# Optimization experiments

Measured on AMD Instinct MI355X. Metric: run time of the kernel, lower is better.

The kernel has to match this reference:

```python
import jax, jax.numpy as jnp
import numpy as np
import jax.lax as lax

H, D, C, CS, NS, OW, PD = 8, 64, 512, 64, 5, 8, 1
MAX_LR = 0.1
KCONV = 4


def short_conv(x, w, b):
    # x: (B,T,Din) -> causal depthwise conv over time
    B, T, Din = x.shape
    xc = jnp.transpose(x, (0, 2, 1))
    xc = jnp.pad(xc, ((0, 0), (0, 0), (KCONV - 1, 0)))
    xc = lax.conv_general_dilated(xc, w, window_strides=(1,), padding='VALID',
                                  dimension_numbers=('NCW', 'OIW', 'NCW'),
                                  feature_group_count=Din)
    xc = xc + b[:, jnp.newaxis]
    return jnp.transpose(xc, (0, 2, 1))


def linear_scan(h_init, gates, inputs):
    # h_t = gate_t * h_{t-1} + input_t ; gates: (B,cs,H), inputs: (B,cs,H,...)
    extra = inputs.ndim - gates.ndim
    g = gates.reshape(gates.shape + (1,) * extra)
    first = g[:, 0:1] * h_init[:, jnp.newaxis] + inputs[:, 0:1]
    mod_in = jnp.concatenate([first, inputs[:, 1:]], axis=1)
    mod_g = jnp.concatenate([jnp.zeros_like(g[:, 0:1]), g[:, 1:]], axis=1)

    def assoc(a, bb):
        ga, xa = a
        gb, xb = bb
        return (ga * gb, gb * xa + xb)

    _, h_all = lax.associative_scan(assoc, (mod_g, mod_in), axis=1)
    return h_all, h_all[:, -1]


def omega_aggregate(u, gamma, w):
    cs = u.shape[1]
    cum = jnp.cumsum(gamma * u, axis=1)
    if w >= cs:
        return cum
    shifted = jnp.concatenate([jnp.zeros_like(cum[:, :w]), cum[:, :-w]], axis=1)
    return cum - shifted


def polar_express(S, steps):
    # Newton-Schulz quintic orthogonalization (Muon/Polar-Express coefficients)
    a, b, c = 3.4445, -4.7750, 2.0315
    n = jnp.sqrt(jnp.sum(S * S, axis=(-2, -1), keepdims=True))
    X = S / (n * 1.01 + 1e-7)
    for _ in range(steps):
        A = X @ jnp.swapaxes(X, -2, -1)
        X = a * X + (b * A + c * (A @ A)) @ X
    return X


def rms_norm(x):
    ms = jnp.mean(x * x, axis=-1, keepdims=True)
    return x * lax.rsqrt(ms + 1e-6)


def atlas_forward(x, Wq, Wk, Wv, Wproj, conv_q_w, conv_q_b, conv_k_w, conv_k_b,
                  conv_v_w, conv_v_b, ga_w, ga_b, ge_w, ge_b, gt_w, gt_b,
                  gg_w, gg_b, poly_coeffs, ln_gamma, W1_init, rg_w):
    B, T, _ = x.shape
    q = short_conv(x @ Wq.T, conv_q_w, conv_q_b).reshape(B, T, H, D)
    k = short_conv(x @ Wk.T, conv_k_w, conv_k_b).reshape(B, T, H, D)
    v = short_conv(x @ Wv.T, conv_v_w, conv_v_b).reshape(B, T, H, D)

    def phi(z):
        r = poly_coeffs[0] * z
        zp = z
        for i in range(1, PD):
            zp = zp * z
            r = r + poly_coeffs[i] * zp
        return r

    q, k = phi(q), phi(k)

    alpha = jax.nn.sigmoid(x @ ga_w.T + ga_b)          # (B,T,H) memory retention
    eta = MAX_LR * jax.nn.sigmoid(x @ ge_w.T + ge_b)   # learning rate
    theta = jax.nn.sigmoid(x @ gt_w.T + gt_b)          # momentum decay
    gamma = jax.nn.sigmoid(x @ gg_w.T + gg_b)          # omega context gate

    nC = T // CS

    def chunk(z):
        return jnp.moveaxis(z.reshape(B, nC, CS, *z.shape[2:]), 1, 0)

    q_ch, k_ch, v_ch = chunk(q), chunk(k), chunk(v)
    a_ch = chunk(alpha)[..., None]
    e_ch = chunk(eta)[..., None]
    t_ch = chunk(theta)[..., None]
    g_ch = chunk(gamma)[..., None]

    M0 = jnp.broadcast_to(W1_init, (B, H, D, D))
    S0 = jnp.zeros((B, H, D, D), x.dtype)

    def step(carry, inp):
        M, S = carry
        q_c, k_c, v_c, a_c, e_c, t_c, g_c = inp
        pred = jnp.einsum('bhvk,bchk->bchv', M, k_c)
        err = pred - v_c
        u = (2.0 / D) * jnp.einsum('bchv,bchk->bchvk', err, k_c)
        u = omega_aggregate(u, g_c[..., None], OW)
        mom_in = -(e_c[..., None] * u)
        chunk_S, S = linear_scan(S, jnp.squeeze(t_c, -1), mom_in)
        chunk_S_orth = polar_express(chunk_S, NS)
        M_all, M = linear_scan(M, jnp.squeeze(a_c, -1), chunk_S_orth)
        y_c = jnp.einsum('bchvk,bchk->bchv', M_all, q_c)
        return (M, S), y_c

    (_, _), y = lax.scan(step, (M0, S0), (q_ch, k_ch, v_ch, a_ch, e_ch, t_ch, g_ch))
    y = jnp.moveaxis(y, 0, 1).reshape(B, T, H, D)
    y = rms_norm(y) * (1.0 + ln_gamma)
    rg = jax.nn.sigmoid(x @ rg_w.T)          # (B,T,H) retrieve gate
    y = y * rg[..., None]
    return y.reshape(B, T, H * D) @ Wproj.T


def setup_inputs() -> dict:
    key = jax.random.key(0)
    ks = jax.random.split(key, 24)
    B, T = 2, 1024
    Din = H * D

    def lin(k, o, i):
        return jax.random.normal(k, (o, i), jnp.float32) * (1.0 / np.sqrt(i))

    bound = float(np.sqrt(6.0 / (D + D)))
    return dict(
        x=jax.random.normal(ks[0], (B, T, C), jnp.float32),
        Wq=lin(ks[1], Din, C), Wk=lin(ks[2], Din, C), Wv=lin(ks[3], Din, C),
        Wproj=lin(ks[4], C, Din),
        conv_q_w=jax.random.normal(ks[5], (Din, 1, KCONV), jnp.float32) * 0.02,
        conv_q_b=jnp.zeros(Din, jnp.float32),
        conv_k_w=jax.random.normal(ks[6], (Din, 1, KCONV), jnp.float32) * 0.02,
        conv_k_b=jnp.zeros(Din, jnp.float32),
        conv_v_w=jax.random.normal(ks[7], (Din, 1, KCONV), jnp.float32) * 0.02,
        conv_v_b=jnp.zeros(Din, jnp.float32),
        ga_w=lin(ks[8], H, C), ga_b=jnp.zeros(H, jnp.float32),
        ge_w=lin(ks[9], H, C), ge_b=jnp.zeros(H, jnp.float32),
        gt_w=lin(ks[10], H, C), gt_b=jnp.zeros(H, jnp.float32),
        gg_w=lin(ks[11], H, C), gg_b=jnp.zeros(H, jnp.float32),
        poly_coeffs=jnp.ones(PD, jnp.float32),
        ln_gamma=jnp.zeros((H, D), jnp.float32),
        W1_init=jax.random.uniform(ks[12], (H, D, D), jnp.float32, -bound, bound),
        rg_w=lin(ks[13], H, C),
    )


def reference(x, Wq, Wk, Wv, Wproj, conv_q_w, conv_q_b, conv_k_w, conv_k_b,
              conv_v_w, conv_v_b, ga_w, ga_b, ge_w, ge_b, gt_w, gt_b,
              gg_w, gg_b, poly_coeffs, ln_gamma, W1_init, rg_w):
    return atlas_forward(x, Wq, Wk, Wv, Wproj, conv_q_w, conv_q_b, conv_k_w,
                         conv_k_b, conv_v_w, conv_v_b, ga_w, ga_b, ge_w, ge_b,
                         gt_w, gt_b, gg_w, gg_b, poly_coeffs, ln_gamma,
                         W1_init, rg_w)
```

## Files before the change

kernel.cpp:

```cpp
#include <hip/hip_runtime.h>

#define B_ 2
#define T_ 1024
#define H_ 8
#define D_ 64
#define PPAD 68

typedef __attribute__((ext_vector_type(8))) short s8v;
typedef __attribute__((ext_vector_type(4))) short s4v;
typedef __attribute__((ext_vector_type(4))) float f4v;

__device__ __forceinline__ short f2bf(float f) {
  unsigned u = __float_as_uint(f);
  u += 0x7fffu + ((u >> 16) & 1u);
  return (short)(u >> 16);
}
__device__ __forceinline__ float bf2f(short s) {
  return __uint_as_float(((unsigned)(unsigned short)s) << 16);
}
__device__ __forceinline__ float sigm(float v) { return 1.0f / (1.0f + __expf(-v)); }

#define MFMA(a, b, c) __builtin_amdgcn_mfma_f32_16x16x32_bf16((a), (b), (c), 0, 0, 0)

__global__ __launch_bounds__(256) void gemm_bt(const float* __restrict__ A,
    const float* __restrict__ Bw, float* __restrict__ Co,
    int M, int N, int K) {
  __shared__ short Ash[64][40], Asl[64][40];
  __shared__ short Bsh[64][40], Bsl[64][40];
  const int tid = threadIdx.x;
  const int lane = tid & 63;
  const int wv = tid >> 6;
  const int wr = (wv >> 1) * 32;
  const int wc = (wv & 1) * 32;
  const int m0 = blockIdx.x * 64;
  const int n0 = blockIdx.y * 64;
  const int ldr = tid >> 2;
  const int ldc = (tid & 3) * 8;
  const int l15 = lane & 15;
  const int kq = (lane >> 4) * 8;
  f4v acc[2][2];
#pragma unroll
  for (int i = 0; i < 2; ++i)
#pragma unroll
    for (int j = 0; j < 2; ++j)
#pragma unroll
      for (int r = 0; r < 4; ++r) acc[i][j][r] = 0.0f;
  const float* ap = A + (size_t)(m0 + ldr) * K + ldc;
  const float* bp = Bw + (size_t)(n0 + ldr) * K + ldc;
  for (int kt = 0; kt < K; kt += 32) {
    float4 av0 = *(const float4*)(ap + kt);
    float4 av1 = *(const float4*)(ap + kt + 4);
    float4 bv0 = *(const float4*)(bp + kt);
    float4 bv1 = *(const float4*)(bp + kt + 4);
    float af[8] = {av0.x, av0.y, av0.z, av0.w, av1.x, av1.y, av1.z, av1.w};
    float bf[8] = {bv0.x, bv0.y, bv0.z, bv0.w, bv1.x, bv1.y, bv1.z, bv1.w};
    s8v ah, al, bh, bl;
#pragma unroll
    for (int i = 0; i < 8; ++i) {
      short h = f2bf(af[i]); ah[i] = h; al[i] = f2bf(af[i] - bf2f(h));
      h = f2bf(bf[i]); bh[i] = h; bl[i] = f2bf(bf[i] - bf2f(h));
    }
    __syncthreads();
    *(s8v*)&Ash[ldr][ldc] = ah; *(s8v*)&Asl[ldr][ldc] = al;
    *(s8v*)&Bsh[ldr][ldc] = bh; *(s8v*)&Bsl[ldr][ldc] = bl;
    __syncthreads();
    s8v a0h = *(const s8v*)&Ash[wr + l15][kq];
    s8v a1h = *(const s8v*)&Ash[wr + 16 + l15][kq];
    s8v b0h = *(const s8v*)&Bsh[wc + l15][kq];
    s8v b1h = *(const s8v*)&Bsh[wc + 16 + l15][kq];
    s8v a0l = *(const s8v*)&Asl[wr + l15][kq];
    s8v a1l = *(const s8v*)&Asl[wr + 16 + l15][kq];
    s8v b0l = *(const s8v*)&Bsl[wc + l15][kq];
    s8v b1l = *(const s8v*)&Bsl[wc + 16 + l15][kq];
    acc[0][0] = MFMA(a0h, b0h, acc[0][0]);
    acc[0][1] = MFMA(a0h, b1h, acc[0][1]);
    acc[1][0] = MFMA(a1h, b0h, acc[1][0]);
    acc[1][1] = MFMA(a1h, b1h, acc[1][1]);
    acc[0][0] = MFMA(a0h, b0l, acc[0][0]);
    acc[0][1] = MFMA(a0h, b1l, acc[0][1]);
    acc[1][0] = MFMA(a1h, b0l, acc[1][0]);
    acc[1][1] = MFMA(a1h, b1l, acc[1][1]);
    acc[0][0] = MFMA(a0l, b0h, acc[0][0]);
    acc[0][1] = MFMA(a0l, b1h, acc[0][1]);
    acc[1][0] = MFMA(a1l, b0h, acc[1][0]);
    acc[1][1] = MFMA(a1l, b1h, acc[1][1]);
  }
#pragma unroll
  for (int m2 = 0; m2 < 2; ++m2)
#pragma unroll
    for (int n2 = 0; n2 < 2; ++n2)
#pragma unroll
      for (int r = 0; r < 4; ++r) {
        int row = m0 + wr + m2 * 16 + (lane >> 4) * 4 + r;
        int col = n0 + wc + n2 * 16 + l15;
        Co[(size_t)row * N + col] = acc[m2][n2][r];
      }
}

__global__ __launch_bounds__(256) void gemm_qkv(const float* __restrict__ A,
    const float* __restrict__ Wq, const float* __restrict__ Wk,
    const float* __restrict__ Wv,
    float* __restrict__ xq, float* __restrict__ xk, float* __restrict__ xv) {
  __shared__ short Ash[64][40], Asl[64][40];
  __shared__ short Bsh[64][40], Bsl[64][40];
  const int sel = blockIdx.y >> 3;
  const float* Bw = sel == 0 ? Wq : (sel == 1 ? Wk : Wv);
  float* Co = sel == 0 ? xq : (sel == 1 ? xk : xv);
  const int tid = threadIdx.x;
  const int lane = tid & 63;
  const int wv = tid >> 6;
  const int wr = (wv >> 1) * 32;
  const int wc = (wv & 1) * 32;
  const int m0 = blockIdx.x * 64;
  const int n0 = (blockIdx.y & 7) * 64;
  const int ldr = tid >> 2;
  const int ldc = (tid & 3) * 8;
  const int l15 = lane & 15;
  const int kq = (lane >> 4) * 8;
  f4v acc[2][2];
#pragma unroll
  for (int i = 0; i < 2; ++i)
#pragma unroll
    for (int j = 0; j < 2; ++j)
#pragma unroll
      for (int r = 0; r < 4; ++r) acc[i][j][r] = 0.0f;
  const float* ap = A + (size_t)(m0 + ldr) * 512 + ldc;
  const float* bp = Bw + (size_t)(n0 + ldr) * 512 + ldc;
  for (int kt = 0; kt < 512; kt += 32) {
    float4 av0 = *(const float4*)(ap + kt);
    float4 av1 = *(const float4*)(ap + kt + 4);
    float4 bv0 = *(const float4*)(bp + kt);
    float4 bv1 = *(const float4*)(bp + kt + 4);
    float af[8] = {av0.x, av0.y, av0.z, av0.w, av1.x, av1.y, av1.z, av1.w};
    float bf[8] = {bv0.x, bv0.y, bv0.z, bv0.w, bv1.x, bv1.y, bv1.z, bv1.w};
    s8v ah, al, bh, bl;
#pragma unroll
    for (int i = 0; i < 8; ++i) {
      short h = f2bf(af[i]); ah[i] = h; al[i] = f2bf(af[i] - bf2f(h));
      h = f2bf(bf[i]); bh[i] = h; bl[i] = f2bf(bf[i] - bf2f(h));
    }
    __syncthreads();
    *(s8v*)&Ash[ldr][ldc] = ah; *(s8v*)&Asl[ldr][ldc] = al;
    *(s8v*)&Bsh[ldr][ldc] = bh; *(s8v*)&Bsl[ldr][ldc] = bl;
    __syncthreads();
    s8v a0h = *(const s8v*)&Ash[wr + l15][kq];
    s8v a1h = *(const s8v*)&Ash[wr + 16 + l15][kq];
    s8v b0h = *(const s8v*)&Bsh[wc + l15][kq];
    s8v b1h = *(const s8v*)&Bsh[wc + 16 + l15][kq];
    s8v a0l = *(const s8v*)&Asl[wr + l15][kq];
    s8v a1l = *(const s8v*)&Asl[wr + 16 + l15][kq];
    s8v b0l = *(const s8v*)&Bsl[wc + l15][kq];
    s8v b1l = *(const s8v*)&Bsl[wc + 16 + l15][kq];
    acc[0][0] = MFMA(a0h, b0h, acc[0][0]);
    acc[0][1] = MFMA(a0h, b1h, acc[0][1]);
    acc[1][0] = MFMA(a1h, b0h, acc[1][0]);
    acc[1][1] = MFMA(a1h, b1h, acc[1][1]);
    acc[0][0] = MFMA(a0h, b0l, acc[0][0]);
    acc[0][1] = MFMA(a0h, b1l, acc[0][1]);
    acc[1][0] = MFMA(a1h, b0l, acc[1][0]);
    acc[1][1] = MFMA(a1h, b1l, acc[1][1]);
    acc[0][0] = MFMA(a0l, b0h, acc[0][0]);
    acc[0][1] = MFMA(a0l, b1h, acc[0][1]);
    acc[1][0] = MFMA(a1l, b0h, acc[1][0]);
    acc[1][1] = MFMA(a1l, b1h, acc[1][1]);
  }
#pragma unroll
  for (int m2 = 0; m2 < 2; ++m2)
#pragma unroll
    for (int n2 = 0; n2 < 2; ++n2)
#pragma unroll
      for (int r = 0; r < 4; ++r) {
        int row = m0 + wr + m2 * 16 + (lane >> 4) * 4 + r;
        int col = n0 + wc + n2 * 16 + l15;
        Co[(size_t)row * 512 + col] = acc[m2][n2][r];
      }
}

__global__ __launch_bounds__(256) void conv3_k(
    const float* __restrict__ xq, const float* __restrict__ xk,
    const float* __restrict__ xv,
    const float* __restrict__ cqw, const float* __restrict__ cqb,
    const float* __restrict__ ckw, const float* __restrict__ ckb,
    const float* __restrict__ cvw, const float* __restrict__ cvb,
    const float* __restrict__ pc,
    float* __restrict__ qb, float* __restrict__ kb, float* __restrict__ vb) {
  const int s = blockIdx.x >> 12;
  const int idx = ((blockIdx.x & 4095) << 8) + threadIdx.x;
  const float* in = s == 0 ? xq : (s == 1 ? xk : xv);
  const float* w  = s == 0 ? cqw : (s == 1 ? ckw : cvw);
  const float* bs = s == 0 ? cqb : (s == 1 ? ckb : cvb);
  float* o        = s == 0 ? qb : (s == 1 ? kb : vb);
  const int d = idx & 511;
  const int bt = idx >> 9;
  const int t = bt & (T_ - 1);
  float acc = bs[d];
#pragma unroll
  for (int j = 0; j < 4; ++j) {
    int tt = t - 3 + j;
    if (tt >= 0) acc += w[d * 4 + j] * in[(size_t)(bt - 3 + j) * 512 + d];
  }
  float sc = (s < 2) ? pc[0] : 1.0f;
  o[idx] = sc * acc;
}

__global__ __launch_bounds__(256) void gates_k(const float* __restrict__ x,
    const float* __restrict__ gaw, const float* __restrict__ gab,
    const float* __restrict__ gew, const float* __restrict__ geb,
    const float* __restrict__ gtw, const float* __restrict__ gtb,
    const float* __restrict__ ggw, const float* __restrict__ ggb,
    const float* __restrict__ rgw,
    float* __restrict__ alpha, float* __restrict__ eta,
    float* __restrict__ theta, float* __restrict__ gam, float* __restrict__ rg) {
  int wv = threadIdx.x >> 6, lane = threadIdx.x & 63;
  int bt = blockIdx.x * 4 + wv;
  float xr[8];
#pragma unroll
  for (int i = 0; i < 8; ++i) xr[i] = x[(size_t)bt * 512 + i * 64 + lane];
  for (int h = 0; h < 8; ++h) {
    float s0 = 0, s1 = 0, s2 = 0, s3 = 0, s4 = 0;
#pragma unroll
    for (int i = 0; i < 8; ++i) {
      float xv = xr[i];
      int o = h * 512 + i * 64 + lane;
      s0 += xv * gaw[o];
      s1 += xv * gew[o];
      s2 += xv * gtw[o];
      s3 += xv * ggw[o];
      s4 += xv * rgw[o];
    }
#pragma unroll
    for (int off = 32; off >= 1; off >>= 1) {
      s0 += __shfl_xor(s0, off);
      s1 += __shfl_xor(s1, off);
      s2 += __shfl_xor(s2, off);
      s3 += __shfl_xor(s3, off);
      s4 += __shfl_xor(s4, off);
    }
    if (lane == 0) {
      size_t o = (size_t)bt * 8 + h;
      alpha[o] = sigm(s0 + gab[h]);
      eta[o]   = 0.1f * sigm(s1 + geb[h]);
      theta[o] = sigm(s2 + gtb[h]);
      gam[o]   = sigm(s3 + ggb[h]);
      rg[o]    = sigm(s4);
    }
  }
}

__global__ __launch_bounds__(256) void init_carry(const float* __restrict__ w1,
    float* __restrict__ Mc, float* __restrict__ Sc) {
  int idx = blockIdx.x * 256 + threadIdx.x;
  Mc[idx] = w1[idx & 32767];
  Sc[idx] = 0.0f;
}

__global__ __launch_bounds__(256) void chunk_a(
    const float* __restrict__ kb, const float* __restrict__ vb,
    const float* __restrict__ eta, const float* __restrict__ theta,
    const float* __restrict__ gam,
    const float* __restrict__ Mc, float* __restrict__ Sc,
    float* __restrict__ chS, int ci) {
  __shared__ float KT[64][65];
  __shared__ float errl[4][68];
  __shared__ float Ml[4][64];
  __shared__ float ge_[64], gt_[64], gg_[64];
  const int tid = threadIdx.x;
  const int bh = blockIdx.x >> 4;
  const int vs = blockIdx.x & 15;
  const int b = bh >> 3, h = bh & 7;
  const int v0 = vs * 4;
  const int t0 = ci * 64;
  const int lane = tid & 63, q4 = tid >> 6;
  for (int it = 0; it < 16; ++it) {
    int c = it * 4 + q4;
    KT[lane][c] = kb[((size_t)(b * T_ + t0 + c) * H_ + h) * 64 + lane];
  }
  if (tid < 64) {
    size_t gi = (size_t)(b * T_ + t0 + tid) * H_ + h;
    ge_[tid] = eta[gi]; gt_[tid] = theta[gi]; gg_[tid] = gam[gi];
  }
  Ml[q4][lane] = Mc[((size_t)bh * 64 + v0 + q4) * 64 + lane];
  __syncthreads();
  {
    int c = lane, vr = q4;
    float p = 0.0f;
#pragma unroll
    for (int k2 = 0; k2 < 64; ++k2) p += KT[k2][c] * Ml[vr][k2];
    float vv = vb[((size_t)(b * T_ + t0 + c) * H_ + h) * 64 + v0 + vr];
    errl[vr][c] = p - vv;
  }
  __syncthreads();
  {
    const int kk = lane, vr = q4, v = v0 + vr;
    float S = Sc[((size_t)bh * 64 + v) * 64 + kk];
    float ring[8];
    float cum = 0.0f;
    float* out = chS + ((size_t)(b << 6) * 8 + h) * 4096 + (size_t)v * 64 + kk;
    for (int c8 = 0; c8 < 8; ++c8) {
#pragma unroll
      for (int j = 0; j < 8; ++j) {
        int c = c8 * 8 + j;
        float u = 0.03125f * errl[vr][c] * KT[kk][c];
        float gu = gg_[c] * u;
        cum += gu;
        if (c8 > 0) cum -= ring[j];
        ring[j] = gu;
        float mom = -ge_[c] * cum;
        S = gt_[c] * S + mom;
        out[(size_t)c * 32768] = S;
      }
    }
    Sc[((size_t)bh * 64 + v) * 64 + kk] = S;
  }
}

__device__ __forceinline__ s8v ld8(const short* p) {
  s4v lo = *(const s4v*)p;
  s4v hi = *(const s4v*)(p + 4);
  s8v r;
  r[0] = lo[0]; r[1] = lo[1]; r[2] = lo[2]; r[3] = lo[3];
  r[4] = hi[0]; r[5] = hi[1]; r[6] = hi[2]; r[7] = hi[3];
  return r;
}

__device__ __forceinline__ void mm8(const short (*Ah)[PPAD], const short (*Al)[PPAD],
    const short (*Bh)[PPAD], const short (*Bl)[PPAD],
    int wr, int wc, int l15, int kq, int sp, f4v acc[2]) {
#pragma unroll
  for (int kt = 0; kt < 64; kt += 32) {
    s8v ah = ld8(&Ah[wr + l15][kt + kq]);
    s8v b0h = ld8(&Bh[wc + l15][kt + kq]);
    s8v b1h = ld8(&Bh[wc + 16 + l15][kt + kq]);
    acc[0] = MFMA(ah, b0h, acc[0]);
    acc[1] = MFMA(ah, b1h, acc[1]);
    if (sp) {
      s8v al_ = ld8(&Al[wr + l15][kt + kq]);
      s8v b0l = ld8(&Bl[wc + l15][kt + kq]);
      s8v b1l = ld8(&Bl[wc + 16 + l15][kt + kq]);
      acc[0] = MFMA(ah, b0l, acc[0]);
      acc[1] = MFMA(ah, b1l, acc[1]);
      acc[0] = MFMA(al_, b0h, acc[0]);
      acc[1] = MFMA(al_, b1h, acc[1]);
    }
  }
}

__global__ __launch_bounds__(512, 6) void polar_k(float* __restrict__ cs) {
  __shared__ short Xh[64][PPAD], Xl[64][PPAD];
  __shared__ short XTh[64][PPAD], XTl[64][PPAD];
  __shared__ short Zh[64][PPAD], Zl[64][PPAD];
  __shared__ float red[8];
  const int tid = threadIdx.x;
  const int lane = tid & 63;
  const int wv = tid >> 6;
  const int wr = (wv >> 1) * 16;
  const int wc = (wv & 1) * 32;
  const int l15 = lane & 15;
  const int q4 = lane >> 4;
  const int kq = q4 * 8;
  const int rr0 = wr + q4 * 4;
  float* base = cs + (size_t)blockIdx.x * 4096;
  float xr[2][4];
  float ss = 0.0f;
#pragma unroll
  for (int n2 = 0; n2 < 2; ++n2)
#pragma unroll
    for (int r = 0; r < 4; ++r) {
      float v = base[(rr0 + r) * 64 + wc + n2 * 16 + l15];
      xr[n2][r] = v;
      ss += v * v;
    }
#pragma unroll
  for (int off = 32; off >= 1; off >>= 1) ss += __shfl_xor(ss, off);
  if (lane == 0) red[wv] = ss;
  __syncthreads();
  float tot = red[0] + red[1] + red[2] + red[3] + red[4] + red[5] + red[6] + red[7];
  float scale = 1.0f / (sqrtf(tot) * 1.01f + 1e-7f);
#pragma unroll
  for (int n2 = 0; n2 < 2; ++n2) {
    const int cc = wc + n2 * 16 + l15;
    s4v hv, lv;
#pragma unroll
    for (int r = 0; r < 4; ++r) {
      float xv = xr[n2][r] * scale;
      xr[n2][r] = xv;
      short hh = f2bf(xv);
      short ll = f2bf(xv - bf2f(hh));
      hv[r] = hh; lv[r] = ll;
      Xh[rr0 + r][cc] = hh;
      Xl[rr0 + r][cc] = ll;
    }
    *(s4v*)&XTh[cc][rr0] = hv;
    *(s4v*)&XTl[cc][rr0] = lv;
  }
  __syncthreads();

  for (int it = 0; it < 5; ++it) {
    const int sp = (it < 4);
    f4v at[2];
#pragma unroll
    for (int n2 = 0; n2 < 2; ++n2)
#pragma unroll
      for (int r = 0; r < 4; ++r) at[n2][r] = 0.0f;
    mm8(XTh, XTl, XTh, XTl, wr, wc, l15, kq, sp, at);
#pragma unroll
    for (int n2 = 0; n2 < 2; ++n2) {
      const int cc = wc + n2 * 16 + l15;
      s4v hv, lv;
#pragma unroll
      for (int r = 0; r < 4; ++r) {
        float a = at[n2][r];
        short hh = f2bf(a);
        hv[r] = hh; lv[r] = f2bf(a - bf2f(hh));
      }
      *(s4v*)&Zh[cc][rr0] = hv;
      if (sp) *(s4v*)&Zl[cc][rr0] = lv;
    }
    __syncthreads();
    f4v a2[2];
#pragma unroll
    for (int n2 = 0; n2 < 2; ++n2)
#pragma unroll
      for (int r = 0; r < 4; ++r) a2[n2][r] = 0.0f;
    mm8(Zh, Zl, Zh, Zl, wr, wc, l15, kq, sp, a2);
    float zt[2][4];
#pragma unroll
    for (int n2 = 0; n2 < 2; ++n2)
#pragma unroll
      for (int r = 0; r < 4; ++r)
        zt[n2][r] = -4.7750f * at[n2][r] + 2.0315f * a2[n2][r];
    __syncthreads();
#pragma unroll
    for (int n2 = 0; n2 < 2; ++n2) {
      const int cc = wc + n2 * 16 + l15;
      s4v hv, lv;
#pragma unroll
      for (int r = 0; r < 4; ++r) {
        float zv = zt[n2][r];
        short hh = f2bf(zv);
        hv[r] = hh; lv[r] = f2bf(zv - bf2f(hh));
      }
      *(s4v*)&Zh[cc][rr0] = hv;
      if (sp) *(s4v*)&Zl[cc][rr0] = lv;
    }
    __syncthreads();
    f4v q3[2];
#pragma unroll
    for (int n2 = 0; n2 < 2; ++n2)
#pragma unroll
      for (int r = 0; r < 4; ++r) q3[n2][r] = 0.0f;
    mm8(Xh, Xl, Zh, Zl, wr, wc, l15, kq, sp, q3);
#pragma unroll
    for (int n2 = 0; n2 < 2; ++n2)
#pragma unroll
      for (int r = 0; r < 4; ++r)
        xr[n2][r] = 3.4445f * xr[n2][r] + q3[n2][r];
    if (it < 4) {
      __syncthreads();
      const int slo = (it < 3);
#pragma unroll
      for (int n2 = 0; n2 < 2; ++n2) {
        const int cc = wc + n2 * 16 + l15;
        s4v hv, lv;
#pragma unroll
        for (int r = 0; r < 4; ++r) {
          float xv = xr[n2][r];
          short hh = f2bf(xv);
          short ll = f2bf(xv - bf2f(hh));
          hv[r] = hh; lv[r] = ll;
          Xh[rr0 + r][cc] = hh;
          if (slo) Xl[rr0 + r][cc] = ll;
        }
        *(s4v*)&XTh[cc][rr0] = hv;
        if (slo) *(s4v*)&XTl[cc][rr0] = lv;
      }
      __syncthreads();
    }
  }
#pragma unroll
  for (int n2 = 0; n2 < 2; ++n2)
#pragma unroll
    for (int r = 0; r < 4; ++r)
      base[(rr0 + r) * 64 + wc + n2 * 16 + l15] = xr[n2][r];
}

__global__ __launch_bounds__(256) void chunk_ca(
    const float* __restrict__ qb, const float* __restrict__ kb,
    const float* __restrict__ vb,
    const float* __restrict__ alpha, const float* __restrict__ eta,
    const float* __restrict__ theta, const float* __restrict__ gam,
    float* __restrict__ Mc, float* __restrict__ Sc,
    float* __restrict__ chS, float* __restrict__ yb, int ci) {
  __shared__ float KT[64][65];
  __shared__ float errl[4][68];
  __shared__ float Ml[4][64];
  __shared__ float ge_[64], gt_[64], gg_[64];
  const int tid = threadIdx.x, lane = tid & 63, w = tid >> 6;
  const int bh = blockIdx.x >> 4, vs = blockIdx.x & 15;
  const int b = bh >> 3, h = bh & 7;
  const int v0 = vs * 4, v = v0 + w;
  const int t0 = ci * 64;
  float M = Mc[((size_t)bh * 64 + v) * 64 + lane];
  const float* op = chS + ((size_t)(b << 6) * 8 + h) * 4096 + (size_t)v * 64 + lane;
  const float* qp = qb + ((size_t)(b * T_ + t0) * 8 + h) * 64 + lane;
  const float* ap = alpha + (size_t)(b * T_ + t0) * 8 + h;
  float* yp = yb + ((size_t)(b * T_ + t0) * 8 + h) * 64 + v;
  float o0 = op[0], o1 = op[32768];
  float q0 = qp[0], q1 = qp[512];
  float a0 = ap[0], a1 = ap[8];
  for (int c = 0; c < 64; c += 2) {
    float o2 = 0.f, o3 = 0.f, q2 = 0.f, q3 = 0.f, a2 = 0.f, a3 = 0.f;
    if (c < 62) {
      o2 = op[(size_t)(c + 2) * 32768]; o3 = op[(size_t)(c + 3) * 32768];
      q2 = qp[(c + 2) * 512];           q3 = qp[(c + 3) * 512];
      a2 = ap[(c + 2) * 8];             a3 = ap[(c + 3) * 8];
    }
    M = a0 * M + o0;
    float p0 = M * q0;
    M = a1 * M + o1;
    float p1 = M * q1;
#pragma unroll
    for (int off = 32; off >= 1; off >>= 1) {
      p0 += __shfl_xor(p0, off);
      p1 += __shfl_xor(p1, off);
    }
    if (lane == 0) {
      yp[(size_t)c * 512] = p0;
      yp[(size_t)(c + 1) * 512] = p1;
    }
    o0 = o2; o1 = o3; q0 = q2; q1 = q3; a0 = a2; a1 = a3;
  }
  Mc[((size_t)bh * 64 + v) * 64 + lane] = M;
  if (ci == 15) return;
  const int t1 = t0 + 64;
  Ml[w][lane] = M;
  for (int it = 0; it < 16; ++it) {
    int c = it * 4 + w;
    KT[lane][c] = kb[((size_t)(b * T_ + t1 + c) * 8 + h) * 64 + lane];
  }
  if (tid < 64) {
    size_t gi = (size_t)(b * T_ + t1 + tid) * 8 + h;
    ge_[tid] = eta[gi]; gt_[tid] = theta[gi]; gg_[tid] = gam[gi];
  }
  __syncthreads();
  {
    int c = lane, vr = w;
    float pr = 0.0f;
#pragma unroll
    for (int k2 = 0; k2 < 64; ++k2) pr += KT[k2][c] * Ml[vr][k2];
    float vv = vb[((size_t)(b * T_ + t1 + c) * 8 + h) * 64 + v0 + vr];
    errl[vr][c] = pr - vv;
  }
  __syncthreads();
  {
    const int kk = lane, vr = w, vv2 = v0 + vr;
    float S = Sc[((size_t)bh * 64 + vv2) * 64 + kk];
    float ring[8];
    float cum = 0.0f;
    float* out = chS + ((size_t)(b << 6) * 8 + h) * 4096 + (size_t)vv2 * 64 + kk;
    for (int c8 = 0; c8 < 8; ++c8) {
#pragma unroll
      for (int j = 0; j < 8; ++j) {
        int c = c8 * 8 + j;
        float u = 0.03125f * errl[vr][c] * KT[kk][c];
        float gu = gg_[c] * u;
        cum += gu;
        if (c8 > 0) cum -= ring[j];
        ring[j] = gu;
        float mom = -ge_[c] * cum;
        S = gt_[c] * S + mom;
        out[(size_t)c * 32768] = S;
      }
    }
    Sc[((size_t)bh * 64 + vv2) * 64 + kk] = S;
  }
}

__global__ __launch_bounds__(256) void norm_k(const float* __restrict__ yb,
    const float* __restrict__ lng, const float* __restrict__ rg,
    float* __restrict__ yn) {
  const int lane = threadIdx.x & 63;
  const int gw = blockIdx.x * 4 + (threadIdx.x >> 6);
  const int h = gw & 7;
  const int bt = gw >> 3;
  float y = yb[(size_t)gw * 64 + lane];
  float s = y * y;
#pragma unroll
  for (int off = 32; off >= 1; off >>= 1) s += __shfl_xor(s, off);
  float r = rsqrtf(s * (1.0f / 64.0f) + 1e-6f);
  yn[(size_t)gw * 64 + lane] = y * r * (1.0f + lng[h * 64 + lane]) * rg[(size_t)bt * 8 + h];
}

extern "C" void kernel_launch(void* const* d_in, const int* in_sizes, int n_in,
                              void* d_out, int out_size, void* d_ws, size_t ws_size,
                              hipStream_t stream) {
  (void)in_sizes; (void)n_in; (void)out_size; (void)ws_size;
  const float* x   = (const float*)d_in[0];
  const float* Wq  = (const float*)d_in[1];
  const float* Wk  = (const float*)d_in[2];
  const float* Wv  = (const float*)d_in[3];
  const float* Wpr = (const float*)d_in[4];
  const float* cqw = (const float*)d_in[5];
  const float* cqb = (const float*)d_in[6];
  const float* ckw = (const float*)d_in[7];
  const float* ckb = (const float*)d_in[8];
  const float* cvw = (const float*)d_in[9];
  const float* cvb = (const float*)d_in[10];
  const float* gaw = (const float*)d_in[11];
  const float* gab = (const float*)d_in[12];
  const float* gew = (const float*)d_in[13];
  const float* geb = (const float*)d_in[14];
  const float* gtw = (const float*)d_in[15];
  const float* gtb = (const float*)d_in[16];
  const float* ggw = (const float*)d_in[17];
  const float* ggb = (const float*)d_in[18];
  const float* pc  = (const float*)d_in[19];
  const float* lng = (const float*)d_in[20];
  const float* w1  = (const float*)d_in[21];
  const float* rgw = (const float*)d_in[22];
  float* outp = (float*)d_out;

  float* chS = (float*)d_ws;
  float* xq = chS;
  float* xk = chS + 1048576;
  float* xv = chS + 2 * 1048576;
  float* yn = chS;
  char* wp = (char*)d_ws + (size_t)16 * 1024 * 1024;
  auto alloc = [&](size_t bytes) {
    char* p = wp;
    wp += (bytes + 255) & ~(size_t)255;
    return p;
  };
  const size_t BT = (size_t)B_ * T_;
  float* qb = (float*)alloc(BT * 512 * 4);
  float* kb = (float*)alloc(BT * 512 * 4);
  float* vb = (float*)alloc(BT * 512 * 4);
  float* yb = (float*)alloc(BT * 512 * 4);
  float* alpha = (float*)alloc(BT * 8 * 4);
  float* eta   = (float*)alloc(BT * 8 * 4);
  float* theta = (float*)alloc(BT * 8 * 4);
  float* gam   = (float*)alloc(BT * 8 * 4);
  float* rg    = (float*)alloc(BT * 8 * 4);
  float* Mc = (float*)alloc((size_t)65536 * 4);
  float* Sc = (float*)alloc((size_t)65536 * 4);

  init_carry<<<dim3(256), dim3(256), 0, stream>>>(w1, Mc, Sc);
  gemm_qkv<<<dim3(32, 24), dim3(256), 0, stream>>>(x, Wq, Wk, Wv, xq, xk, xv);
  conv3_k<<<dim3(12288), dim3(256), 0, stream>>>(xq, xk, xv, cqw, cqb, ckw, ckb,
                                                 cvw, cvb, pc, qb, kb, vb);
  gates_k<<<dim3(512), dim3(256), 0, stream>>>(x, gaw, gab, gew, geb, gtw, gtb,
                                               ggw, ggb, rgw, alpha, eta, theta, gam, rg);
  chunk_a<<<dim3(256), dim3(256), 0, stream>>>(kb, vb, eta, theta, gam, Mc, Sc, chS, 0);
  for (int ci = 0; ci < 16; ++ci) {
    polar_k<<<dim3(1024), dim3(512), 0, stream>>>(chS);
    chunk_ca<<<dim3(256), dim3(256), 0, stream>>>(qb, kb, vb, alpha, eta, theta, gam,
                                                  Mc, Sc, chS, yb, ci);
  }
  norm_k<<<dim3(4096), dim3(256), 0, stream>>>(yb, lng, rg, yn);
  gemm_bt<<<dim3(32, 8), dim3(256), 0, stream>>>(yn, Wpr, outp, 2048, 512, 512);
}
```

Before: 1.274 ms.

## Use 4-wave 32x32 tiles in polar kernel; preload chunk scan inputs into registers

```diff
diff --git a/kernel.cpp b/kernel.cpp
--- a/kernel.cpp
+++ b/kernel.cpp
@@ -323,168 +323,200 @@
   return r;
 }
 
-__device__ __forceinline__ void mm8(const short (*Ah)[PPAD], const short (*Al)[PPAD],
+__device__ __forceinline__ void mm4(const short (*Ah)[PPAD], const short (*Al)[PPAD],
     const short (*Bh)[PPAD], const short (*Bl)[PPAD],
-    int wr, int wc, int l15, int kq, int sp, f4v acc[2]) {
+    int wr, int wc, int l15, int kq, int sp, f4v acc[2][2]) {
 #pragma unroll
   for (int kt = 0; kt < 64; kt += 32) {
-    s8v ah = ld8(&Ah[wr + l15][kt + kq]);
+    s8v a0h = ld8(&Ah[wr + l15][kt + kq]);
+    s8v a1h = ld8(&Ah[wr + 16 + l15][kt + kq]);
     s8v b0h = ld8(&Bh[wc + l15][kt + kq]);
     s8v b1h = ld8(&Bh[wc + 16 + l15][kt + kq]);
-    acc[0] = MFMA(ah, b0h, acc[0]);
-    acc[1] = MFMA(ah, b1h, acc[1]);
+    acc[0][0] = MFMA(a0h, b0h, acc[0][0]);
+    acc[0][1] = MFMA(a0h, b1h, acc[0][1]);
+    acc[1][0] = MFMA(a1h, b0h, acc[1][0]);
+    acc[1][1] = MFMA(a1h, b1h, acc[1][1]);
     if (sp) {
-      s8v al_ = ld8(&Al[wr + l15][kt + kq]);
+      s8v a0l = ld8(&Al[wr + l15][kt + kq]);
+      s8v a1l = ld8(&Al[wr + 16 + l15][kt + kq]);
       s8v b0l = ld8(&Bl[wc + l15][kt + kq]);
       s8v b1l = ld8(&Bl[wc + 16 + l15][kt + kq]);
-      acc[0] = MFMA(ah, b0l, acc[0]);
-      acc[1] = MFMA(ah, b1l, acc[1]);
-      acc[0] = MFMA(al_, b0h, acc[0]);
-      acc[1] = MFMA(al_, b1h, acc[1]);
-    }
-  }
-}
-
-__global__ __launch_bounds__(512, 6) void polar_k(float* __restrict__ cs) {
+      acc[0][0] = MFMA(a0h, b0l, acc[0][0]);
+      acc[0][1] = MFMA(a0h, b1l, acc[0][1]);
+      acc[1][0] = MFMA(a1h, b0l, acc[1][0]);
+      acc[1][1] = MFMA(a1h, b1l, acc[1][1]);
+      acc[0][0] = MFMA(a0l, b0h, acc[0][0]);
+      acc[0][1] = MFMA(a0l, b1h, acc[0][1]);
+      acc[1][0] = MFMA(a1l, b0h, acc[1][0]);
+      acc[1][1] = MFMA(a1l, b1h, acc[1][1]);
+    }
+  }
+}
+
+__global__ __launch_bounds__(256, 3) void polar_k(float* __restrict__ cs) {
   __shared__ short Xh[64][PPAD], Xl[64][PPAD];
   __shared__ short XTh[64][PPAD], XTl[64][PPAD];
   __shared__ short Zh[64][PPAD], Zl[64][PPAD];
-  __shared__ float red[8];
+  __shared__ float red[4];
   const int tid = threadIdx.x;
   const int lane = tid & 63;
-  const int wv = tid >> 6;
-  const int wr = (wv >> 1) * 16;
-  const int wc = (wv & 1) * 32;
+  const int w = tid >> 6;
+  const int wr = (w >> 1) * 32;
+  const int wc = (w & 1) * 32;
   const int l15 = lane & 15;
   const int q4 = lane >> 4;
   const int kq = q4 * 8;
-  const int rr0 = wr + q4 * 4;
   float* base = cs + (size_t)blockIdx.x * 4096;
-  float xr[2][4];
+  float xr[2][2][4];
   float ss = 0.0f;
 #pragma unroll
-  for (int n2 = 0; n2 < 2; ++n2)
-#pragma unroll
-    for (int r = 0; r < 4; ++r) {
-      float v = base[(rr0 + r) * 64 + wc + n2 * 16 + l15];
-      xr[n2][r] = v;
-      ss += v * v;
-    }
+  for (int m2 = 0; m2 < 2; ++m2)
+#pragma unroll
+    for (int n2 = 0; n2 < 2; ++n2)
+#pragma unroll
+      for (int r = 0; r < 4; ++r) {
+        float v = base[(wr + m2 * 16 + q4 * 4 + r) * 64 + wc + n2 * 16 + l15];
+        xr[m2][n2][r] = v;
+        ss += v * v;
+      }
 #pragma unroll
   for (int off = 32; off >= 1; off >>= 1) ss += __shfl_xor(ss, off);
-  if (lane == 0) red[wv] = ss;
+  if (lane == 0) red[w] = ss;
   __syncthreads();
-  float tot = red[0] + red[1] + red[2] + red[3] + red[4] + red[5] + red[6] + red[7];
-  float scale = 1.0f / (sqrtf(tot) * 1.01f + 1e-7f);
-#pragma unroll
-  for (int n2 = 0; n2 < 2; ++n2) {
-    const int cc = wc + n2 * 16 + l15;
-    s4v hv, lv;
-#pragma unroll
-    for (int r = 0; r < 4; ++r) {
-      float xv = xr[n2][r] * scale;
-      xr[n2][r] = xv;
-      short hh = f2bf(xv);
-      short ll = f2bf(xv - bf2f(hh));
-      hv[r] = hh; lv[r] = ll;
-      Xh[rr0 + r][cc] = hh;
-      Xl[rr0 + r][cc] = ll;
-    }
-    *(s4v*)&XTh[cc][rr0] = hv;
-    *(s4v*)&XTl[cc][rr0] = lv;
-  }
+  float scale = 1.0f / (sqrtf(red[0] + red[1] + red[2] + red[3]) * 1.01f + 1e-7f);
+#pragma unroll
+  for (int m2 = 0; m2 < 2; ++m2)
+#pragma unroll
+    for (int n2 = 0; n2 < 2; ++n2) {
+      const int rr0 = wr + m2 * 16 + q4 * 4;
+      const int cc = wc + n2 * 16 + l15;
+      s4v hv, lv;
+#pragma unroll
+      for (int r = 0; r < 4; ++r) {
+        float xv = xr[m2][n2][r] * scale;
+        xr[m2][n2][r] = xv;
+        short hh = f2bf(xv);
+        short ll = f2bf(xv - bf2f(hh));
+        hv[r] = hh; lv[r] = ll;
+        Xh[rr0 + r][cc] = hh;
+        Xl[rr0 + r][cc] = ll;
+      }
+      *(s4v*)&XTh[cc][rr0] = hv;
+      *(s4v*)&XTl[cc][rr0] = lv;
+    }
   __syncthreads();
 
   for (int it = 0; it < 5; ++it) {
     const int sp = (it < 4);
-    f4v at[2];
-#pragma unroll
-    for (int n2 = 0; n2 < 2; ++n2)
-#pragma unroll
-      for (int r = 0; r < 4; ++r) at[n2][r] = 0.0f;
-    mm8(XTh, XTl, XTh, XTl, wr, wc, l15, kq, sp, at);
-#pragma unroll
-    for (int n2 = 0; n2 < 2; ++n2) {
-      const int cc = wc + n2 * 16 + l15;
-      s4v hv, lv;
-#pragma unroll
-      for (int r = 0; r < 4; ++r) {
-        float a = at[n2][r];
-        short hh = f2bf(a);
-        hv[r] = hh; lv[r] = f2bf(a - bf2f(hh));
-      }
-      *(s4v*)&Zh[cc][rr0] = hv;
-      if (sp) *(s4v*)&Zl[cc][rr0] = lv;
-    }
+    f4v at[2][2];
+#pragma unroll
+    for (int m2 = 0; m2 < 2; ++m2)
+#pragma unroll
+      for (int n2 = 0; n2 < 2; ++n2)
+#pragma unroll
+        for (int r = 0; r < 4; ++r) at[m2][n2][r] = 0.0f;
+    mm4(XTh, XTl, XTh, XTl, wr, wc, l15, kq, sp, at);
+#pragma unroll
+    for (int m2 = 0; m2 < 2; ++m2)
+#pragma unroll
+      for (int n2 = 0; n2 < 2; ++n2) {
+        const int rr0 = wr + m2 * 16 + q4 * 4;
+        const int cc = wc + n2 * 16 + l15;
+        s4v hv, lv;
+#pragma unroll
+        for (int r = 0; r < 4; ++r) {
+          float a = at[m2][n2][r];
+          short hh = f2bf(a);
+          hv[r] = hh; lv[r] = f2bf(a - bf2f(hh));
+        }
+        *(s4v*)&Zh[cc][rr0] = hv;
+        if (sp) *(s4v*)&Zl[cc][rr0] = lv;
+      }
     __syncthreads();
-    f4v a2[2];
-#pragma unroll
-    for (int n2 = 0; n2 < 2; ++n2)
-#pragma unroll
-      for (int r = 0; r < 4; ++r) a2[n2][r] = 0.0f;
-    mm8(Zh, Zl, Zh, Zl, wr, wc, l15, kq, sp, a2);
-    float zt[2][4];
-#pragma unroll
-    for (int n2 = 0; n2 < 2; ++n2)
-#pragma unroll
-      for (int r = 0; r < 4; ++r)
-        zt[n2][r] = -4.7750f * at[n2][r] + 2.0315f * a2[n2][r];
+    f4v a2[2][2];
+#pragma unroll
+    for (int m2 = 0; m2 < 2; ++m2)
+#pragma unroll
+      for (int n2 = 0; n2 < 2; ++n2)
+#pragma unroll
+        for (int r = 0; r < 4; ++r) a2[m2][n2][r] = 0.0f;
+    mm4(Zh, Zl, Zh, Zl, wr, wc, l15, kq, sp, a2);
+    float zt[2][2][4];
+#pragma unroll
+    for (int m2 = 0; m2 < 2; ++m2)
+#pragma unroll
+      for (int n2 = 0; n2 < 2; ++n2)
+#pragma unroll
+        for (int r = 0; r < 4; ++r)
+          zt[m2][n2][r] = -4.7750f * at[m2][n2][r] + 2.0315f * a2[m2][n2][r];
     __syncthreads();
 #pragma unroll
-    for (int n2 = 0; n2 < 2; ++n2) {
-      const int cc = wc + n2 * 16 + l15;
-      s4v hv, lv;
-#pragma unroll
-      for (int r = 0; r < 4; ++r) {
-        float zv = zt[n2][r];
-        short hh = f2bf(zv);
-        hv[r] = hh; lv[r] = f2bf(zv - bf2f(hh));
-      }
-      *(s4v*)&Zh[cc][rr0] = hv;
-      if (sp) *(s4v*)&Zl[cc][rr0] = lv;
-    }
+    for (int m2 = 0; m2 < 2; ++m2)
+#pragma unroll
+      for (int n2 = 0; n2 < 2; ++n2) {
+        const int rr0 = wr + m2 * 16 + q4 * 4;
+        const int cc = wc + n2 * 16 + l15;
+        s4v hv, lv;
+#pragma unroll
+        for (int r = 0; r < 4; ++r) {
+          float zv = zt[m2][n2][r];
+          short hh = f2bf(zv);
+          hv[r] = hh; lv[r] = f2bf(zv - bf2f(hh));
+        }
+        *(s4v*)&Zh[cc][rr0] = hv;
+        if (sp) *(s4v*)&Zl[cc][rr0] = lv;
+      }
     __syncthreads();
-    f4v q3[2];
-#pragma unroll
-    for (int n2 = 0; n2 < 2; ++n2)
-#pragma unroll
-      for (int r = 0; r < 4; ++r) q3[n2][r] = 0.0f;
-    mm8(Xh, Xl, Zh, Zl, wr, wc, l15, kq, sp, q3);
-#pragma unroll
-    for (int n2 = 0; n2 < 2; ++n2)
-#pragma unroll
-      for (int r = 0; r < 4; ++r)
-        xr[n2][r] = 3.4445f * xr[n2][r] + q3[n2][r];
+    f4v q3[2][2];
+#pragma unroll
+    for (int m2 = 0; m2 < 2; ++m2)
+#pragma unroll
+      for (int n2 = 0; n2 < 2; ++n2)
+#pragma unroll
+        for (int r = 0; r < 4; ++r) q3[m2][n2][r] = 0.0f;
+    mm4(Xh, Xl, Zh, Zl, wr, wc, l15, kq, sp, q3);
+#pragma unroll
+    for (int m2 = 0; m2 < 2; ++m2)
+#pragma unroll
+      for (int n2 = 0; n2 < 2; ++n2)
+#pragma unroll
+        for (int r = 0; r < 4; ++r)
+          xr[m2][n2][r] = 3.4445f * xr[m2][n2][r] + q3[m2][n2][r];
     if (it < 4) {
       __syncthreads();
       const int slo = (it < 3);
 #pragma unroll
-      for (int n2 = 0; n2 < 2; ++n2) {
-        const int cc = wc + n2 * 16 + l15;
-        s4v hv, lv;
-#pragma unroll
-        for (int r = 0; r < 4; ++r) {
-          float xv = xr[n2][r];
-          short hh = f2bf(xv);
-          short ll = f2bf(xv - bf2f(hh));
-          hv[r] = hh; lv[r] = ll;
-          Xh[rr0 + r][cc] = hh;
-          if (slo) Xl[rr0 + r][cc] = ll;
+      for (int m2 = 0; m2 < 2; ++m2)
+#pragma unroll
+        for (int n2 = 0; n2 < 2; ++n2) {
+          const int rr0 = wr + m2 * 16 + q4 * 4;
+          const int cc = wc + n2 * 16 + l15;
+          s4v hv, lv;
+#pragma unroll
+          for (int r = 0; r < 4; ++r) {
+            float xv = xr[m2][n2][r];
+            short hh = f2bf(xv);
+            short ll = f2bf(xv - bf2f(hh));
+            hv[r] = hh; lv[r] = ll;
+            Xh[rr0 + r][cc] = hh;
+            if (slo) Xl[rr0 + r][cc] = ll;
+          }
+          *(s4v*)&XTh[cc][rr0] = hv;
+          if (slo) *(s4v*)&XTl[cc][rr0] = lv;
         }
-        *(s4v*)&XTh[cc][rr0] = hv;
-        if (slo) *(s4v*)&XTl[cc][rr0] = lv;
-      }
       __syncthreads();
     }
   }
 #pragma unroll
-  for (int n2 = 0; n2 < 2; ++n2)
-#pragma unroll
-    for (int r = 0; r < 4; ++r)
-      base[(rr0 + r) * 64 + wc + n2 * 16 + l15] = xr[n2][r];
-}
-
-__global__ __launch_bounds__(256) void chunk_ca(
+  for (int m2 = 0; m2 < 2; ++m2)
+#pragma unroll
+    for (int n2 = 0; n2 < 2; ++n2)
+#pragma unroll
+      for (int r = 0; r < 4; ++r)
+        base[(wr + m2 * 16 + q4 * 4 + r) * 64 + wc + n2 * 16 + l15] = xr[m2][n2][r];
+}
+
+__global__ __launch_bounds__(256, 1) void chunk_ca(
     const float* __restrict__ qb, const float* __restrict__ kb,
     const float* __restrict__ vb,
     const float* __restrict__ alpha, const float* __restrict__ eta,
@@ -503,32 +535,20 @@
   float M = Mc[((size_t)bh * 64 + v) * 64 + lane];
   const float* op = chS + ((size_t)(b << 6) * 8 + h) * 4096 + (size_t)v * 64 + lane;
   const float* qp = qb + ((size_t)(b * T_ + t0) * 8 + h) * 64 + lane;
-  const float* ap = alpha + (size_t)(b * T_ + t0) * 8 + h;
   float* yp = yb + ((size_t)(b * T_ + t0) * 8 + h) * 64 + v;
-  float o0 = op[0], o1 = op[32768];
-  float q0 = qp[0], q1 = qp[512];
-  float a0 = ap[0], a1 = ap[8];
-  for (int c = 0; c < 64; c += 2) {
-    float o2 = 0.f, o3 = 0.f, q2 = 0.f, q3 = 0.f, a2 = 0.f, a3 = 0.f;
-    if (c < 62) {
-      o2 = op[(size_t)(c + 2) * 32768]; o3 = op[(size_t)(c + 3) * 32768];
-      q2 = qp[(c + 2) * 512];           q3 = qp[(c + 3) * 512];
-      a2 = ap[(c + 2) * 8];             a3 = ap[(c + 3) * 8];
-    }
-    M = a0 * M + o0;
-    float p0 = M * q0;
-    M = a1 * M + o1;
-    float p1 = M * q1;
-#pragma unroll
-    for (int off = 32; off >= 1; off >>= 1) {
-      p0 += __shfl_xor(p0, off);
-      p1 += __shfl_xor(p1, off);
-    }
-    if (lane == 0) {
-      yp[(size_t)c * 512] = p0;
-      yp[(size_t)(c + 1) * 512] = p1;
-    }
-    o0 = o2; o1 = o3; q0 = q2; q1 = q3; a0 = a2; a1 = a3;
+  float av = alpha[(size_t)(b * T_ + t0 + lane) * 8 + h];
+  float ov[64], qv[64];
+#pragma unroll
+  for (int c = 0; c < 64; ++c) ov[c] = op[(size_t)c * 32768];
+#pragma unroll
+  for (int c = 0; c < 64; ++c) qv[c] = qp[(size_t)c * 512];
+#pragma unroll
+  for (int c = 0; c < 64; ++c) {
+    M = __builtin_fmaf(__shfl(av, c), M, ov[c]);
+    float p = M * qv[c];
+#pragma unroll
+    for (int off = 32; off >= 1; off >>= 1) p += __shfl_xor(p, off);
+    if (lane == 0) yp[(size_t)c * 512] = p;
   }
   Mc[((size_t)bh * 64 + v) * 64 + lane] = M;
   if (ci == 15) return;
@@ -652,7 +672,7 @@
                                                ggw, ggb, rgw, alpha, eta, theta, gam, rg);
   chunk_a<<<dim3(256), dim3(256), 0, stream>>>(kb, vb, eta, theta, gam, Mc, Sc, chS, 0);
   for (int ci = 0; ci < 16; ++ci) {
-    polar_k<<<dim3(1024), dim3(512), 0, stream>>>(chS);
+    polar_k<<<dim3(1024), dim3(256), 0, stream>>>(chS);
     chunk_ca<<<dim3(256), dim3(256), 0, stream>>>(qb, kb, vb, alpha, eta, theta, gam,
                                                   Mc, Sc, chS, yb, ci);
   }
```

Measured after the change: 1.258 ms. About the same (-1.3%).
